# Optimization experiments

Hardware: AMD Instinct MI355X
Metric: run time of the kernel (lower is better)

## Reference

```python
import jax, jax.numpy as jnp
import numpy as np


def _sdpa(q, k, v):
    # q: [B,H,Sq,D], k/v: [B,H,Sk,D]; torch F.scaled_dot_product_attention default scale
    scale = 1.0 / np.sqrt(q.shape[-1]).astype(np.float32)
    logits = jnp.einsum('bhqd,bhkd->bhqk', q, k) * scale
    w = jax.nn.softmax(logits, axis=-1)
    return jnp.einsum('bhqk,bhkd->bhqd', w, v)


def setup_inputs() -> dict:
    key = jax.random.key(0)
    ks = jax.random.split(key, 8)
    B2, S, C = 4, 1024, 1280  # full batch = [noise; ref], SDXL-like 32x32 latent
    Bh = B2 // 2
    w_init = 1.0 / np.sqrt(C).astype(np.float32)
    return {
        'hidden_states': jax.random.normal(ks[0], (B2, S, C), jnp.float32),
        'mask_ref': jax.random.uniform(ks[1], (Bh, S, 1), jnp.float32),
        'Wq': jax.random.normal(ks[2], (C, C), jnp.float32) * w_init,
        'Wk': jax.random.normal(ks[3], (C, C), jnp.float32) * w_init,
        'Wv': jax.random.normal(ks[4], (C, C), jnp.float32) * w_init,
        'Wo': jax.random.normal(ks[5], (C, C), jnp.float32) * w_init,
        'bo': jnp.zeros((C,), jnp.float32),
        'heads': 20,
    }


def reference(hidden_states, mask_ref, Wq, Wk, Wv, Wo, bo, heads):
    module_scale = 1.0  # self.scale
    B2, S, C = hidden_states.shape
    B = B2 // 2
    H = heads
    D = C // H
    noise = hidden_states[:B]
    ref = hidden_states[B:]

    # NOTE: faithful to source quirk: query uses the FULL 2B batch, then is
    # viewed as (B, 2S, H, D) -> q has query length 2S.
    query = jnp.einsum('bsc,oc->bso', hidden_states, Wq)  # [2B,S,C]
    q = query.reshape(B, 2 * S, H, D).transpose(0, 2, 1, 3)  # [B,H,2S,D]

    # background branch: self-attention over noise tokens
    k_bg = jnp.einsum('bsc,oc->bso', noise, Wk).reshape(B, S, H, D).transpose(0, 2, 1, 3)
    v_bg = jnp.einsum('bsc,oc->bso', noise, Wv).reshape(B, S, H, D).transpose(0, 2, 1, 3)
    hidden_bg = _sdpa(q, k_bg, v_bg).transpose(0, 2, 1, 3).reshape(B, 2 * S, C)

    # face branch: cross-attention onto reference tokens, K/V gated by mask_ref
    gate = mask_ref.reshape(B, 1, S, 1)  # [B,1,Sk,1]
    k_face = jnp.einsum('bsc,oc->bso', ref, Wk).reshape(B, S, H, D).transpose(0, 2, 1, 3) * gate
    v_face = jnp.einsum('bsc,oc->bso', ref, Wv).reshape(B, S, H, D).transpose(0, 2, 1, 3) * gate
    hidden_face = _sdpa(q, k_face, v_face).transpose(0, 2, 1, 3).reshape(B, 2 * S, C)

    merged = hidden_bg + hidden_face * module_scale  # mask is None -> additive merge
    out = jnp.einsum('bsc,oc->bso', merged, Wo) + bo  # to_out[0]; dropout is identity
    return out
```

## Files before the change

### kernel.cpp

```cpp
#include <hip/hip_runtime.h>
#include <hip/hip_bf16.h>

typedef __bf16 bf16;
typedef __bf16 bf16x8 __attribute__((ext_vector_type(8)));
typedef __bf16 bf16x4 __attribute__((ext_vector_type(4)));
typedef float f32x4 __attribute__((ext_vector_type(4)));

#define CDIM 1280

static __device__ __forceinline__ f32x4 mfma16(bf16x8 a, bf16x8 b, f32x4 c) {
  return __builtin_amdgcn_mfma_f32_16x16x32_bf16(a, b, c, 0, 0, 0);
}

static __device__ __forceinline__ void gload_lds(const bf16* g, bf16* l) {
  __builtin_amdgcn_global_load_lds(
      (const __attribute__((address_space(1))) void*)g,
      (__attribute__((address_space(3))) void*)l, 16, 0, 0);
}

static __device__ __forceinline__ float fexp2(float x) {
#if __has_builtin(__builtin_amdgcn_exp2f)
  return __builtin_amdgcn_exp2f(x);
#else
  return __expf(x * 0.6931471805599453f);
#endif
}

__global__ __launch_bounds__(256) void cvt_all(const float* __restrict__ h,
                                               const float* __restrict__ wq,
                                               const float* __restrict__ wk,
                                               const float* __restrict__ wv,
                                               const float* __restrict__ wo,
                                               bf16* __restrict__ hb, bf16* __restrict__ wqb,
                                               bf16* __restrict__ wkb, bf16* __restrict__ wvb,
                                               bf16* __restrict__ wob) {
  int id = blockIdx.x * 256 + threadIdx.x;
  const float* src; bf16* dst; int off;
  if (id < 1310720) { src = h; dst = hb; off = id; }
  else {
    int t = id - 1310720;
    int w = t / 409600; off = t % 409600;
    src = (w == 0) ? wq : (w == 1) ? wk : (w == 2) ? wv : wo;
    dst = (w == 0) ? wqb : (w == 1) ? wkb : (w == 2) ? wvb : wob;
  }
  float4 v = reinterpret_cast<const float4*>(src)[off];
  bf16x4 o;
  o[0] = (bf16)v.x; o[1] = (bf16)v.y; o[2] = (bf16)v.z; o[3] = (bf16)v.w;
  reinterpret_cast<bf16x4*>(dst)[off] = o;
}

__global__ __launch_bounds__(256) void qkv_gemm(const bf16* __restrict__ X,
                                                const bf16* __restrict__ Wq,
                                                const bf16* __restrict__ Wk,
                                                const bf16* __restrict__ Wv,
                                                const float* __restrict__ mask,
                                                bf16* __restrict__ Qb,
                                                bf16* __restrict__ Kb,
                                                bf16* __restrict__ Vt) {
  __shared__ bf16 SM[2][128 * 64];
  bf16* Al = SM[0];
  bf16* Bl = SM[1];
  const int tid = threadIdx.x, lane = tid & 63, wv = tid >> 6;
  const int lr = lane & 15, lg = lane >> 4;
  const int xb = blockIdx.x, by = blockIdx.y;
  const int wsel = xb / 10;
  const int cb = (xb % 10) * 128;
  const bf16* W = (wsel == 0) ? Wq : (wsel == 1) ? Wk : Wv;
  const int strow = tid >> 3, stchk = tid & 7;
  f32x4 acc[4][4] = {};
  for (int kt = 0; kt < 20; ++kt) {
    __syncthreads();
#pragma unroll
    for (int i = 0; i < 4; ++i) {
      gload_lds(X + (size_t)(by * 128 + i * 32 + strow) * CDIM + kt * 64 + stchk * 8,
                &Al[(i * 256 + tid) * 8]);
      gload_lds(W + (size_t)(cb + i * 32 + strow) * CDIM + kt * 64 + stchk * 8,
                &Bl[(i * 256 + tid) * 8]);
    }
    __syncthreads();
#pragma unroll
    for (int kk = 0; kk < 2; ++kk) {
      bf16x8 a[4], b[4];
#pragma unroll
      for (int i = 0; i < 4; ++i) {
        a[i] = *(const bf16x8*)&Al[((wv >> 1) * 64 + i * 16 + lr) * 64 + kk * 32 + lg * 8];
        b[i] = *(const bf16x8*)&Bl[((wv & 1) * 64 + i * 16 + lr) * 64 + kk * 32 + lg * 8];
      }
#pragma unroll
      for (int i = 0; i < 4; ++i)
#pragma unroll
        for (int j = 0; j < 4; ++j)
          acc[i][j] = mfma16(a[i], b[j], acc[i][j]);
    }
  }
  if (wsel == 2) {
    __syncthreads();
    bf16* T = &SM[0][0];
#pragma unroll
    for (int i = 0; i < 4; ++i)
#pragma unroll
      for (int r = 0; r < 4; ++r) {
        const int lrow = (wv >> 1) * 64 + i * 16 + lg * 4 + r;
        const int row = by * 128 + lrow;
        const float g = (row >= 2048) ? mask[row - 2048] : 1.0f;
        const int rb = lrow >> 6, kpos = lrow & 63;
        const int jp = (kpos & 32) + ((kpos >> 2) & 3) * 8 + ((kpos >> 4) & 1) * 4 + (kpos & 3);
#pragma unroll
        for (int j = 0; j < 4; ++j) {
          const int col = (wv & 1) * 64 + j * 16 + lr;
          T[col * 128 + ((rb * 64 + jp) ^ ((col & 7) << 3))] = (bf16)(acc[i][j][r] * g);
        }
      }
    __syncthreads();
#pragma unroll
    for (int q = 0; q < 8; ++q) {
      const int col = (tid >> 4) + q * 16;
      const int rc = tid & 15, rb = rc >> 3, rc8 = rc & 7;
      bf16x8 vv = *(const bf16x8*)&T[col * 128 + rb * 64 + ((rc8 ^ (col & 7)) << 3)];
      const int gcol = cb + col, hh = gcol >> 6, d = gcol & 63;
      const int kb64 = by * 2 + rb;
      const int br = kb64 >> 5, bb = (kb64 >> 4) & 1, kt = kb64 & 15;
      *(bf16x8*)&Vt[(size_t)(((br * 40 + bb * 20 + hh) * 16 + kt) * 64 + d) * 64 + rc8 * 8] = vv;
    }
  } else {
    const int rbase = by * 128 + (wv >> 1) * 64;
    const int cbase = cb + (wv & 1) * 64;
    bf16* Y = (wsel == 0) ? Qb : Kb;
    const bool gated = (wsel == 1);
#pragma unroll
    for (int i = 0; i < 4; ++i)
#pragma unroll
      for (int r = 0; r < 4; ++r) {
        const int row = rbase + i * 16 + lg * 4 + r;
        const float g = (gated && row >= 2048) ? mask[row - 2048] : 1.0f;
#pragma unroll
        for (int j = 0; j < 4; ++j)
          Y[(size_t)row * CDIM + cbase + j * 16 + lr] = (bf16)(acc[i][j][r] * g);
      }
  }
}

__global__ __launch_bounds__(256) void attn_kernel(const bf16* __restrict__ Q,
                                                   const bf16* __restrict__ K,
                                                   const bf16* __restrict__ Vt,
                                                   bf16* __restrict__ Mg) {
  __shared__ bf16 Kl[2][64 * 64];
  __shared__ bf16 Vl[2][64 * 64];
  const int tid = threadIdx.x, lane = tid & 63, wv = tid >> 6;
  const int lr = lane & 15, lg = lane >> 4;
  const int bid = blockIdx.x;
  const int sb = (bid & 7) * 160 + (bid >> 3);
  const int qt = sb & 31, hh = (sb >> 5) % 20, b = sb / 640;
  const int qrow = b * 2048 + qt * 64 + wv * 16;
  const int strow = tid >> 3, stchk = tid & 7;
  const int sw = lr & 7;

  const bf16* Kb0 = K + (size_t)(b * 1024) * CDIM + hh * 64;
  const bf16* Vb0 = Vt + (size_t)(b * 20 + hh) * 65536;

  bf16x8 qf0, qf1;
  {
    const float SL2E = 0.125f * 1.4426950408889634f;
    const bf16* qp = Q + (size_t)(qrow + lr) * CDIM + hh * 64 + lg * 8;
    bf16x8 r0 = *(const bf16x8*)qp;
    bf16x8 r1 = *(const bf16x8*)(qp + 32);
#pragma unroll
    for (int j = 0; j < 8; ++j) {
      qf0[j] = (bf16)((float)r0[j] * SL2E);
      qf1[j] = (bf16)((float)r1[j] * SL2E);
    }
  }

  auto stage = [&](int t, int buf) {
    const int br = t >> 4, kt = t & 15;
    const bf16* Kp = Kb0 + (size_t)br * 2048 * CDIM;
    const bf16* Vp = Vb0 + (size_t)br * 40 * 65536;
#pragma unroll
    for (int i = 0; i < 2; ++i) {
      const int row = i * 32 + strow;
      gload_lds(Kp + (size_t)(kt * 64 + row) * CDIM + (stchk ^ (row & 7)) * 8,
                &Kl[buf][(i * 256 + tid) * 8]);
      gload_lds(Vp + kt * 4096 + row * 64 + (stchk ^ (row & 7)) * 8,
                &Vl[buf][(i * 256 + tid) * 8]);
    }
  };

  float m = -INFINITY, l = 0.f;
  f32x4 O[4] = {};
  f32x4 Ofin[4] = {};

  stage(0, 0);
  __syncthreads();

  for (int t = 0; t < 32; ++t) {
    const int cur = t & 1;
    if (t < 31) stage(t + 1, cur ^ 1);

    f32x4 z[4];
    __builtin_amdgcn_s_setprio(1);
#pragma unroll
    for (int kb = 0; kb < 4; ++kb) {
      const int row = kb * 16 + lr;
      bf16x8 k0 = *(const bf16x8*)&Kl[cur][row * 64 + (lg ^ sw) * 8];
      bf16x8 k1 = *(const bf16x8*)&Kl[cur][row * 64 + ((4 + lg) ^ sw) * 8];
      f32x4 zz = {};
      zz = mfma16(k0, qf0, zz);
      zz = mfma16(k1, qf1, zz);
      z[kb] = zz;
    }
    __builtin_amdgcn_s_setprio(0);

    float pm = -INFINITY;
#pragma unroll
    for (int kb = 0; kb < 4; ++kb)
#pragma unroll
      for (int r = 0; r < 4; ++r) pm = fmaxf(pm, z[kb][r]);
    pm = fmaxf(pm, __shfl_xor(pm, 16, 64));
    pm = fmaxf(pm, __shfl_xor(pm, 32, 64));

    float p[16], rs = 0.f;
    if (__all(pm <= m + 8.f)) {
#pragma unroll
      for (int kb = 0; kb < 4; ++kb)
#pragma unroll
        for (int r = 0; r < 4; ++r) {
          float e = fexp2(z[kb][r] - m);
          p[kb * 4 + r] = e; rs += e;
        }
      rs += __shfl_xor(rs, 16, 64);
      rs += __shfl_xor(rs, 32, 64);
      l += rs;
    } else {
      const float mn = fmaxf(m, pm);
      const float al = fexp2(m - mn);
#pragma unroll
      for (int kb = 0; kb < 4; ++kb)
#pragma unroll
        for (int r = 0; r < 4; ++r) {
          float e = fexp2(z[kb][r] - mn);
          p[kb * 4 + r] = e; rs += e;
        }
      rs += __shfl_xor(rs, 16, 64);
      rs += __shfl_xor(rs, 32, 64);
      l = l * al + rs;
      m = mn;
#pragma unroll
      for (int dt = 0; dt < 4; ++dt) {
        O[dt][0] *= al; O[dt][1] *= al; O[dt][2] *= al; O[dt][3] *= al;
      }
    }

    bf16x8 pb0, pb1;
#pragma unroll
    for (int e = 0; e < 8; ++e) { pb0[e] = (bf16)p[e]; pb1[e] = (bf16)p[8 + e]; }

    __builtin_amdgcn_s_setprio(1);
#pragma unroll
    for (int dt = 0; dt < 4; ++dt) {
      const int row = dt * 16 + lr;
      bf16x8 v0 = *(const bf16x8*)&Vl[cur][row * 64 + (lg ^ sw) * 8];
      bf16x8 v1 = *(const bf16x8*)&Vl[cur][row * 64 + ((4 + lg) ^ sw) * 8];
      O[dt] = mfma16(v0, pb0, O[dt]);
      O[dt] = mfma16(v1, pb1, O[dt]);
    }
    __builtin_amdgcn_s_setprio(0);

    if (t == 15 || t == 31) {
      const float invl = 1.0f / l;
#pragma unroll
      for (int dt = 0; dt < 4; ++dt) {
        Ofin[dt][0] += O[dt][0] * invl; Ofin[dt][1] += O[dt][1] * invl;
        Ofin[dt][2] += O[dt][2] * invl; Ofin[dt][3] += O[dt][3] * invl;
      }
      if (t == 15) {
        m = -INFINITY; l = 0.f;
#pragma unroll
        for (int dt = 0; dt < 4; ++dt) O[dt] = f32x4{};
      }
    }
    __syncthreads();
  }

#pragma unroll
  for (int dt = 0; dt < 4; ++dt) {
    bf16x4 o4;
    o4[0] = (bf16)Ofin[dt][0]; o4[1] = (bf16)Ofin[dt][1];
    o4[2] = (bf16)Ofin[dt][2]; o4[3] = (bf16)Ofin[dt][3];
    *(bf16x4*)&Mg[(size_t)(qrow + lr) * CDIM + hh * 64 + dt * 16 + lg * 4] = o4;
  }
}

__global__ __launch_bounds__(256) void out_gemm(const bf16* __restrict__ X,
                                                const bf16* __restrict__ W,
                                                const float* __restrict__ bias,
                                                float* __restrict__ Y) {
  __shared__ bf16 Al[128 * 64];
  __shared__ bf16 Bl[128 * 64];
  const int tid = threadIdx.x, lane = tid & 63, wv = tid >> 6;
  const int lr = lane & 15, lg = lane >> 4;
  const int cb = blockIdx.x * 128, by = blockIdx.y;
  const int strow = tid >> 3, stchk = tid & 7;
  f32x4 acc[4][4] = {};
  for (int kt = 0; kt < 20; ++kt) {
    __syncthreads();
#pragma unroll
    for (int i = 0; i < 4; ++i) {
      gload_lds(X + (size_t)(by * 128 + i * 32 + strow) * CDIM + kt * 64 + stchk * 8,
                &Al[(i * 256 + tid) * 8]);
      gload_lds(W + (size_t)(cb + i * 32 + strow) * CDIM + kt * 64 + stchk * 8,
                &Bl[(i * 256 + tid) * 8]);
    }
    __syncthreads();
#pragma unroll
    for (int kk = 0; kk < 2; ++kk) {
      bf16x8 a[4], b[4];
#pragma unroll
      for (int i = 0; i < 4; ++i) {
        a[i] = *(const bf16x8*)&Al[((wv >> 1) * 64 + i * 16 + lr) * 64 + kk * 32 + lg * 8];
        b[i] = *(const bf16x8*)&Bl[((wv & 1) * 64 + i * 16 + lr) * 64 + kk * 32 + lg * 8];
      }
#pragma unroll
      for (int i = 0; i < 4; ++i)
#pragma unroll
        for (int j = 0; j < 4; ++j)
          acc[i][j] = mfma16(a[i], b[j], acc[i][j]);
    }
  }
  const int rbase = by * 128 + (wv >> 1) * 64;
  const int cbase = cb + (wv & 1) * 64;
#pragma unroll
  for (int i = 0; i < 4; ++i)
#pragma unroll
    for (int r = 0; r < 4; ++r) {
      const int row = rbase + i * 16 + lg * 4 + r;
#pragma unroll
      for (int j = 0; j < 4; ++j) {
        const int col = cbase + j * 16 + lr;
        Y[(size_t)row * CDIM + col] = acc[i][j][r] + bias[col];
      }
    }
}

extern "C" void kernel_launch(void* const* d_in, const int* in_sizes, int n_in,
                              void* d_out, int out_size, void* d_ws, size_t ws_size,
                              hipStream_t stream) {
  const float* hidden = (const float*)d_in[0];
  const float* mask   = (const float*)d_in[1];
  const float* Wq     = (const float*)d_in[2];
  const float* Wk     = (const float*)d_in[3];
  const float* Wv     = (const float*)d_in[4];
  const float* Wo     = (const float*)d_in[5];
  const float* bo     = (const float*)d_in[6];
  float* out = (float*)d_out;

  char* ws = (char*)d_ws;
  bf16* hb  = (bf16*)(ws);
  bf16* wqb = (bf16*)(ws + 10485760);
  bf16* wkb = (bf16*)(ws + 13762560);
  bf16* wvb = (bf16*)(ws + 17039360);
  bf16* wob = (bf16*)(ws + 20316160);
  bf16* Qb  = (bf16*)(ws + 23592960);
  bf16* Kb  = (bf16*)(ws + 34078720);
  bf16* Vt  = (bf16*)(ws + 44564480);
  bf16* Mg  = hb;

  cvt_all<<<dim3(11520), 256, 0, stream>>>(hidden, Wq, Wk, Wv, Wo, hb, wqb, wkb, wvb, wob);
  qkv_gemm<<<dim3(30, 32), 256, 0, stream>>>(hb, wqb, wkb, wvb, mask, Qb, Kb, Vt);
  attn_kernel<<<dim3(1280), 256, 0, stream>>>(Qb, Kb, Vt, Mg);
  out_gemm<<<dim3(10, 32), 256, 0, stream>>>(Mg, wob, bo, out);
}
```

Baseline: 207.0 us.

## Process two query sub-tiles per wave in attention to reuse K/V LDS fragments

Each wave now handles 32 query rows (two 16-row sub-tiles) instead of 16, so every block covers 128 queries and the grid is halved to 640 blocks. The K and V fragments read from LDS, and the staged K/V tiles, are reused across both sub-tiles, which halves K/V global and LDS traffic per query. The cost is more registers per thread (two sets of O accumulators and softmax state) and fewer blocks, which lowers occupancy and may leave the 256 CUs with less than three waves of blocks.

```diff
diff --git a/kernel.cpp b/kernel.cpp
--- a/kernel.cpp
+++ b/kernel.cpp
@@ -149,25 +149,28 @@
   const int tid = threadIdx.x, lane = tid & 63, wv = tid >> 6;
   const int lr = lane & 15, lg = lane >> 4;
   const int bid = blockIdx.x;
-  const int sb = (bid & 7) * 160 + (bid >> 3);
-  const int qt = sb & 31, hh = (sb >> 5) % 20, b = sb / 640;
-  const int qrow = b * 2048 + qt * 64 + wv * 16;
+  const int sb = (bid & 7) * 80 + (bid >> 3);
+  const int qt = sb & 15, hh = (sb >> 4) % 20, b = sb / 320;
+  const int qrow = b * 2048 + qt * 128 + wv * 32;
   const int strow = tid >> 3, stchk = tid & 7;
   const int sw = lr & 7;
 
   const bf16* Kb0 = K + (size_t)(b * 1024) * CDIM + hh * 64;
   const bf16* Vb0 = Vt + (size_t)(b * 20 + hh) * 65536;
 
-  bf16x8 qf0, qf1;
+  bf16x8 qf[2][2];
   {
     const float SL2E = 0.125f * 1.4426950408889634f;
-    const bf16* qp = Q + (size_t)(qrow + lr) * CDIM + hh * 64 + lg * 8;
-    bf16x8 r0 = *(const bf16x8*)qp;
-    bf16x8 r1 = *(const bf16x8*)(qp + 32);
-#pragma unroll
-    for (int j = 0; j < 8; ++j) {
-      qf0[j] = (bf16)((float)r0[j] * SL2E);
-      qf1[j] = (bf16)((float)r1[j] * SL2E);
+#pragma unroll
+    for (int qs = 0; qs < 2; ++qs) {
+      const bf16* qp = Q + (size_t)(qrow + qs * 16 + lr) * CDIM + hh * 64 + lg * 8;
+      bf16x8 r0 = *(const bf16x8*)qp;
+      bf16x8 r1 = *(const bf16x8*)(qp + 32);
+#pragma unroll
+      for (int j = 0; j < 8; ++j) {
+        qf[0][qs][j] = (bf16)((float)r0[j] * SL2E);
+        qf[1][qs][j] = (bf16)((float)r1[j] * SL2E);
+      }
     }
   }
 
@@ -185,9 +188,9 @@
     }
   };
 
-  float m = -INFINITY, l = 0.f;
-  f32x4 O[4] = {};
-  f32x4 Ofin[4] = {};
+  float m_[2] = {-INFINITY, -INFINITY}, l_[2] = {0.f, 0.f};
+  f32x4 O[4][2] = {};
+  f32x4 Ofin[4][2] = {};
 
   stage(0, 0);
   __syncthreads();
@@ -196,63 +199,71 @@
     const int cur = t & 1;
     if (t < 31) stage(t + 1, cur ^ 1);
 
-    f32x4 z[4];
-    __builtin_amdgcn_s_setprio(1);
+    bf16x8 kf[4][2];
 #pragma unroll
     for (int kb = 0; kb < 4; ++kb) {
       const int row = kb * 16 + lr;
-      bf16x8 k0 = *(const bf16x8*)&Kl[cur][row * 64 + (lg ^ sw) * 8];
-      bf16x8 k1 = *(const bf16x8*)&Kl[cur][row * 64 + ((4 + lg) ^ sw) * 8];
-      f32x4 zz = {};
-      zz = mfma16(k0, qf0, zz);
-      zz = mfma16(k1, qf1, zz);
-      z[kb] = zz;
-    }
-    __builtin_amdgcn_s_setprio(0);
-
-    float pm = -INFINITY;
-#pragma unroll
-    for (int kb = 0; kb < 4; ++kb)
-#pragma unroll
-      for (int r = 0; r < 4; ++r) pm = fmaxf(pm, z[kb][r]);
-    pm = fmaxf(pm, __shfl_xor(pm, 16, 64));
-    pm = fmaxf(pm, __shfl_xor(pm, 32, 64));
-
-    float p[16], rs = 0.f;
-    if (__all(pm <= m + 8.f)) {
+      kf[kb][0] = *(const bf16x8*)&Kl[cur][row * 64 + (lg ^ sw) * 8];
+      kf[kb][1] = *(const bf16x8*)&Kl[cur][row * 64 + ((4 + lg) ^ sw) * 8];
+    }
+
+    bf16x8 pb[2][2];
+#pragma unroll
+    for (int qs = 0; qs < 2; ++qs) {
+      f32x4 z[4];
+      __builtin_amdgcn_s_setprio(1);
+#pragma unroll
+      for (int kb = 0; kb < 4; ++kb) {
+        f32x4 zz = {};
+        zz = mfma16(kf[kb][0], qf[0][qs], zz);
+        zz = mfma16(kf[kb][1], qf[1][qs], zz);
+        z[kb] = zz;
+      }
+      __builtin_amdgcn_s_setprio(0);
+
+      float pm = -INFINITY;
 #pragma unroll
       for (int kb = 0; kb < 4; ++kb)
 #pragma unroll
-        for (int r = 0; r < 4; ++r) {
-          float e = fexp2(z[kb][r] - m);
-          p[kb * 4 + r] = e; rs += e;
+        for (int r = 0; r < 4; ++r) pm = fmaxf(pm, z[kb][r]);
+      pm = fmaxf(pm, __shfl_xor(pm, 16, 64));
+      pm = fmaxf(pm, __shfl_xor(pm, 32, 64));
+
+      float p[16], rs = 0.f;
+      if (__all(pm <= m_[qs] + 8.f)) {
+#pragma unroll
+        for (int kb = 0; kb < 4; ++kb)
+#pragma unroll
+          for (int r = 0; r < 4; ++r) {
+            float e = fexp2(z[kb][r] - m_[qs]);
+            p[kb * 4 + r] = e; rs += e;
+          }
+        rs += __shfl_xor(rs, 16, 64);
+        rs += __shfl_xor(rs, 32, 64);
+        l_[qs] += rs;
+      } else {
+        const float mn = fmaxf(m_[qs], pm);
+        const float al = fexp2(m_[qs] - mn);
+#pragma unroll
+        for (int kb = 0; kb < 4; ++kb)
+#pragma unroll
+          for (int r = 0; r < 4; ++r) {
+            float e = fexp2(z[kb][r] - mn);
+            p[kb * 4 + r] = e; rs += e;
+          }
+        rs += __shfl_xor(rs, 16, 64);
+        rs += __shfl_xor(rs, 32, 64);
+        l_[qs] = l_[qs] * al + rs;
+        m_[qs] = mn;
+#pragma unroll
+        for (int dt = 0; dt < 4; ++dt) {
+          O[dt][qs][0] *= al; O[dt][qs][1] *= al;
+          O[dt][qs][2] *= al; O[dt][qs][3] *= al;
         }
-      rs += __shfl_xor(rs, 16, 64);
-      rs += __shfl_xor(rs, 32, 64);
-      l += rs;
-    } else {
-      const float mn = fmaxf(m, pm);
-      const float al = fexp2(m - mn);
-#pragma unroll
-      for (int kb = 0; kb < 4; ++kb)
-#pragma unroll
-        for (int r = 0; r < 4; ++r) {
-          float e = fexp2(z[kb][r] - mn);
-          p[kb * 4 + r] = e; rs += e;
-        }
-      rs += __shfl_xor(rs, 16, 64);
-      rs += __shfl_xor(rs, 32, 64);
-      l = l * al + rs;
-      m = mn;
-#pragma unroll
-      for (int dt = 0; dt < 4; ++dt) {
-        O[dt][0] *= al; O[dt][1] *= al; O[dt][2] *= al; O[dt][3] *= al;
-      }
-    }
-
-    bf16x8 pb0, pb1;
-#pragma unroll
-    for (int e = 0; e < 8; ++e) { pb0[e] = (bf16)p[e]; pb1[e] = (bf16)p[8 + e]; }
+      }
+#pragma unroll
+      for (int e = 0; e < 8; ++e) { pb[qs][0][e] = (bf16)p[e]; pb[qs][1][e] = (bf16)p[8 + e]; }
+    }
 
     __builtin_amdgcn_s_setprio(1);
 #pragma unroll
@@ -260,34 +271,45 @@
       const int row = dt * 16 + lr;
       bf16x8 v0 = *(const bf16x8*)&Vl[cur][row * 64 + (lg ^ sw) * 8];
       bf16x8 v1 = *(const bf16x8*)&Vl[cur][row * 64 + ((4 + lg) ^ sw) * 8];
-      O[dt] = mfma16(v0, pb0, O[dt]);
-      O[dt] = mfma16(v1, pb1, O[dt]);
+#pragma unroll
+      for (int qs = 0; qs < 2; ++qs) {
+        O[dt][qs] = mfma16(v0, pb[qs][0], O[dt][qs]);
+        O[dt][qs] = mfma16(v1, pb[qs][1], O[dt][qs]);
+      }
     }
     __builtin_amdgcn_s_setprio(0);
 
     if (t == 15 || t == 31) {
-      const float invl = 1.0f / l;
-#pragma unroll
-      for (int dt = 0; dt < 4; ++dt) {
-        Ofin[dt][0] += O[dt][0] * invl; Ofin[dt][1] += O[dt][1] * invl;
-        Ofin[dt][2] += O[dt][2] * invl; Ofin[dt][3] += O[dt][3] * invl;
+#pragma unroll
+      for (int qs = 0; qs < 2; ++qs) {
+        const float invl = 1.0f / l_[qs];
+#pragma unroll
+        for (int dt = 0; dt < 4; ++dt) {
+          Ofin[dt][qs][0] += O[dt][qs][0] * invl; Ofin[dt][qs][1] += O[dt][qs][1] * invl;
+          Ofin[dt][qs][2] += O[dt][qs][2] * invl; Ofin[dt][qs][3] += O[dt][qs][3] * invl;
+        }
       }
       if (t == 15) {
-        m = -INFINITY; l = 0.f;
-#pragma unroll
-        for (int dt = 0; dt < 4; ++dt) O[dt] = f32x4{};
-      }
-    }
-    __syncthreads();
-  }
-
-#pragma unroll
-  for (int dt = 0; dt < 4; ++dt) {
-    bf16x4 o4;
-    o4[0] = (bf16)Ofin[dt][0]; o4[1] = (bf16)Ofin[dt][1];
-    o4[2] = (bf16)Ofin[dt][2]; o4[3] = (bf16)Ofin[dt][3];
-    *(bf16x4*)&Mg[(size_t)(qrow + lr) * CDIM + hh * 64 + dt * 16 + lg * 4] = o4;
-  }
+#pragma unroll
+        for (int qs = 0; qs < 2; ++qs) { m_[qs] = -INFINITY; l_[qs] = 0.f; }
+#pragma unroll
+        for (int dt = 0; dt < 4; ++dt)
+#pragma unroll
+          for (int qs = 0; qs < 2; ++qs) O[dt][qs] = f32x4{};
+      }
+    }
+    __syncthreads();
+  }
+
+#pragma unroll
+  for (int dt = 0; dt < 4; ++dt)
+#pragma unroll
+    for (int qs = 0; qs < 2; ++qs) {
+      bf16x4 o4;
+      o4[0] = (bf16)Ofin[dt][qs][0]; o4[1] = (bf16)Ofin[dt][qs][1];
+      o4[2] = (bf16)Ofin[dt][qs][2]; o4[3] = (bf16)Ofin[dt][qs][3];
+      *(bf16x4*)&Mg[(size_t)(qrow + qs * 16 + lr) * CDIM + hh * 64 + dt * 16 + lg * 4] = o4;
+    }
 }
 
 __global__ __launch_bounds__(256) void out_gemm(const bf16* __restrict__ X,
@@ -366,6 +388,6 @@
 
   cvt_all<<<dim3(11520), 256, 0, stream>>>(hidden, Wq, Wk, Wv, Wo, hb, wqb, wkb, wvb, wob);
   qkv_gemm<<<dim3(30, 32), 256, 0, stream>>>(hb, wqb, wkb, wvb, mask, Qb, Kb, Vt);
-  attn_kernel<<<dim3(1280), 256, 0, stream>>>(Qb, Kb, Vt, Mg);
+  attn_kernel<<<dim3(640), 256, 0, stream>>>(Qb, Kb, Vt, Mg);
   out_gemm<<<dim3(10, 32), 256, 0, stream>>>(Mg, wob, bo, out);
 }
```

Result: slower. 228.6 us (+10.5%).
